# Kernel optimization log

Measured on AMD Instinct MI355X. Metric: run time of the kernel, lower is better.

## Reference

```python
import jax, jax.numpy as jnp
import numpy as np

N0, N1, N2, N3 = 65536, 16384, 4096, 1024
S = 9  # 3x3 kernel -> 9 selections (self + 8 directions)


def _edges(key, n):
    # each node has S incoming edges, one per selection
    src = jax.random.randint(key, (n * S,), 0, n)
    dst = jnp.repeat(jnp.arange(n), S)
    sel = jnp.tile(jnp.arange(S), n)
    return src, dst, sel


def setup_inputs() -> dict:
    key = jax.random.key(0)
    ks = jax.random.split(key, 40)
    inp = {}
    inp["x"] = jax.random.normal(ks[0], (N0, 3), jnp.float32)
    sizes = [N0, N1, N2, N3]
    for l, n in enumerate(sizes):
        src, dst, sel = _edges(ks[1 + l], n)
        inp[f"src{l}"] = src
        inp[f"dst{l}"] = dst
        inp[f"sel{l}"] = sel
        inp[f"interp{l}"] = jax.random.uniform(ks[5 + l], (n * S,), jnp.float32)
    inp["clus0"] = jnp.arange(N0) // 4
    inp["clus1"] = jnp.arange(N1) // 4
    inp["clus2"] = jnp.arange(N2) // 4
    dims = [(3, 3), (3, 64), (64, 64), (64, 128), (128, 128), (128, 256), (256, 256), (256, 256), (256, 256), (256, 512)]
    for i, (ci, co) in enumerate(dims):
        kw = ks[10 + 2 * i]
        kb = ks[11 + 2 * i]
        if i == 0:  # conv1 is kernel_size=1 -> single weight matrix
            inp["W1"] = jax.random.normal(kw, (ci, co), jnp.float32) / np.sqrt(ci).astype(np.float32)
        else:
            inp[f"W{i + 1}"] = jax.random.normal(kw, (S, ci, co), jnp.float32) / np.sqrt(S * ci).astype(np.float32)
        inp[f"b{i + 1}"] = jax.random.normal(kb, (co,), jnp.float32) * 0.01
    return inp


def _sel_conv(x, src, dst, sel, interp, W, b):
    # message = interp * x[src]; routed to (dst, selection) bucket; per-selection weight
    n = x.shape[0]
    msg = x[src] * interp[:, None]                                  # [E, Cin]
    agg = jax.ops.segment_sum(msg, dst * S + sel, num_segments=n * S)
    agg = agg.reshape(n, S, -1)                                     # [N, S, Cin]
    return jnp.einsum('nsi,sio->no', agg, W) + b


def reference(x, src0, dst0, sel0, interp0, src1, dst1, sel1, interp1,
              src2, dst2, sel2, interp2, src3, dst3, sel3, interp3,
              clus0, clus1, clus2,
              W1, b1, W2, b2, W3, b3, W4, b4, W5, b5,
              W6, b6, W7, b7, W8, b8, W9, b9, W10, b10):
    relu = jax.nn.relu
    out = x @ W1 + b1                                              # conv1 (1x1), no relu
    r11 = relu(_sel_conv(out, src0, dst0, sel0, interp0, W2, b2))
    r12 = relu(_sel_conv(r11, src0, dst0, sel0, interp0, W3, b3))
    p1 = jax.ops.segment_max(r12, clus0, num_segments=N1)
    r21 = relu(_sel_conv(p1, src1, dst1, sel1, interp1, W4, b4))
    r22 = relu(_sel_conv(r21, src1, dst1, sel1, interp1, W5, b5))
    p2 = jax.ops.segment_max(r22, clus1, num_segments=N2)
    r31 = relu(_sel_conv(p2, src2, dst2, sel2, interp2, W6, b6))
    r32 = relu(_sel_conv(r31, src2, dst2, sel2, interp2, W7, b7))
    r33 = relu(_sel_conv(r32, src2, dst2, sel2, interp2, W8, b8))
    r34 = relu(_sel_conv(r33, src2, dst2, sel2, interp2, W9, b9))
    p3 = jax.ops.segment_max(r34, clus2, num_segments=N3)
    r41 = relu(_sel_conv(p3, src3, dst3, sel3, interp3, W10, b10))
    return (r11, r12, p1, r21, r22, p2, r31, r32, r33, r34, p3, r41)
```

## Files before the change

### kernel.cpp

```cpp
#include <hip/hip_runtime.h>
#include <hip/hip_bf16.h>
#include <cstddef>


#define S9 9

typedef __attribute__((ext_vector_type(8))) _Float16 f16x8;
typedef __attribute__((ext_vector_type(4))) float f32x4;

__device__ __forceinline__ unsigned short f2h(float f) {
    _Float16 h = (_Float16)f;
    unsigned short u;
    __builtin_memcpy(&u, &h, 2);
    return u;
}

__device__ void wt_tile(const float* __restrict__ in, unsigned short* __restrict__ out,
                        int K, int N, int t, float (*sm)[33]) {
    const int ktiles = K >> 6, ntiles = N >> 5;
    const int per = ktiles * ntiles;
    const int s = t / per;
    const int rem = t - s * per;
    const int kt = rem % ktiles, nt = rem / ktiles;
    const int k0 = kt * 64, n0 = nt * 32;
    const float* ip = in + (size_t)s * K * N;
    unsigned short* op = out + (size_t)s * N * K;
    const int tx = threadIdx.x & 31;
    const int ty = threadIdx.x >> 5;
#pragma unroll
    for (int r = ty; r < 64; r += 8)
        sm[r][tx] = ip[(size_t)(k0 + r) * N + n0 + tx];
    __syncthreads();
#pragma unroll
    for (int r = ty; r < 32; r += 8) {
        unsigned v = (unsigned)f2h(sm[2 * tx][r]) |
                     ((unsigned)f2h(sm[2 * tx + 1][r]) << 16);
        *(unsigned*)&op[(size_t)(n0 + r) * K + k0 + 2 * tx] = v;
    }
}

__global__ __launch_bounds__(256) void wt_all(
    const float* __restrict__ W2, const float* __restrict__ W3,
    const float* __restrict__ W4, const float* __restrict__ W5,
    const float* __restrict__ W6, const float* __restrict__ W7,
    const float* __restrict__ W8, const float* __restrict__ W9,
    const float* __restrict__ W10,
    unsigned short* o2, unsigned short* o3, unsigned short* o4,
    unsigned short* o5, unsigned short* o6, unsigned short* o7,
    unsigned short* o8, unsigned short* o9, unsigned short* o10) {
    __shared__ float sm[64][33];
    int b = blockIdx.x;
    if (b == 0) {
        for (int idx = threadIdx.x; idx < 64 * 32; idx += 256) {
            const int n = idx >> 5, k = idx & 31;
            o2[n * 32 + k] = (k < 27) ? f2h(W2[k * 64 + n]) : (unsigned short)0;
        }
        return;
    }
    b -= 1;
    if (b < 18)  { wt_tile(W3,  o3,  64,  64,  b, sm); return; }  b -= 18;
    if (b < 36)  { wt_tile(W4,  o4,  64,  128, b, sm); return; }  b -= 36;
    if (b < 72)  { wt_tile(W5,  o5,  128, 128, b, sm); return; }  b -= 72;
    if (b < 144) { wt_tile(W6,  o6,  128, 256, b, sm); return; }  b -= 144;
    if (b < 288) { wt_tile(W7,  o7,  256, 256, b, sm); return; }  b -= 288;
    if (b < 288) { wt_tile(W8,  o8,  256, 256, b, sm); return; }  b -= 288;
    if (b < 288) { wt_tile(W9,  o9,  256, 256, b, sm); return; }  b -= 288;
    wt_tile(W10, o10, 256, 512, b, sm);
}

__global__ void pool4_dual(const float* __restrict__ in, float* __restrict__ outf,
                           _Float16* __restrict__ outh, int total4, int C4) {
    int idx = blockIdx.x * blockDim.x + threadIdx.x;
    if (idx >= total4) return;
    int j = idx / C4;
    int c4 = idx - j * C4;
    const float4* base = (const float4*)in;
    float4 a = base[(size_t)(4 * j + 0) * C4 + c4];
    float4 b = base[(size_t)(4 * j + 1) * C4 + c4];
    float4 c = base[(size_t)(4 * j + 2) * C4 + c4];
    float4 d = base[(size_t)(4 * j + 3) * C4 + c4];
    float4 m;
    m.x = fmaxf(fmaxf(a.x, b.x), fmaxf(c.x, d.x));
    m.y = fmaxf(fmaxf(a.y, b.y), fmaxf(c.y, d.y));
    m.z = fmaxf(fmaxf(a.z, b.z), fmaxf(c.z, d.z));
    m.w = fmaxf(fmaxf(a.w, b.w), fmaxf(c.w, d.w));
    ((float4*)outf)[(size_t)j * C4 + c4] = m;
    uint2 h;
    h.x = (unsigned)f2h(m.x) | ((unsigned)f2h(m.y) << 16);
    h.y = (unsigned)f2h(m.z) | ((unsigned)f2h(m.w) << 16);
    *(uint2*)&outh[((size_t)j * C4 + c4) * 4] = h;
}

template <int BM, int WR, int WC, int MR, int NR>
__global__ __launch_bounds__(256) void selconv_k27(
    const float* __restrict__ x, const int* __restrict__ src,
    const float* __restrict__ interp, const float* __restrict__ W1,
    const float* __restrict__ b1, const _Float16* __restrict__ Wt2,
    const float* __restrict__ bias, float* __restrict__ out,
    _Float16* __restrict__ outh) {
    constexpr int COUT = 64;
    constexpr int LDA = 40;
    __shared__ _Float16 As[BM * LDA];

    const int tid = threadIdx.x;
    const int wave = tid >> 6;
    const int lane = tid & 63;
    const int wr = wave / WC;
    const int wc = wave % WC;
    const int node0 = blockIdx.x * BM;
    const int lm = lane & 15;
    const int kq = lane >> 4;

    const float w00 = W1[0], w01 = W1[1], w02 = W1[2];
    const float w10 = W1[3], w11 = W1[4], w12 = W1[5];
    const float w20 = W1[6], w21 = W1[7], w22 = W1[8];
    const float c0 = b1[0], c1 = b1[1], c2 = b1[2];

    for (int c = tid; c < BM * 5; c += 256) {
        const int ln = c / 5;
        As[ln * LDA + 27 + (c - ln * 5)] = (_Float16)0.f;
    }
    for (int c = tid; c < BM * S9; c += 256) {
        const int ln = c / S9;
        const int s = c - ln * S9;
        const int e = (node0 + ln) * S9 + s;
        const float t = interp[e];
        const float* xr = &x[(size_t)src[e] * 3];
        const float x0 = xr[0], x1 = xr[1], x2 = xr[2];
        const float y0 = fmaf(x0, w00, fmaf(x1, w10, fmaf(x2, w20, c0)));
        const float y1 = fmaf(x0, w01, fmaf(x1, w11, fmaf(x2, w21, c1)));
        const float y2 = fmaf(x0, w02, fmaf(x1, w12, fmaf(x2, w22, c2)));
        As[ln * LDA + s * 3 + 0] = (_Float16)(t * y0);
        As[ln * LDA + s * 3 + 1] = (_Float16)(t * y1);
        As[ln * LDA + s * 3 + 2] = (_Float16)(t * y2);
    }
    __syncthreads();

    f32x4 acc[MR][NR];
    f16x8 bfr[NR];
#pragma unroll
    for (int f = 0; f < NR; ++f) {
        const int col = wc * NR * 16 + f * 16 + lm;
        bfr[f] = *(const f16x8*)(Wt2 + col * 32 + kq * 8);
        const float bv = bias[col];
#pragma unroll
        for (int i = 0; i < MR; ++i) {
            acc[i][f][0] = bv; acc[i][f][1] = bv; acc[i][f][2] = bv; acc[i][f][3] = bv;
        }
    }
#pragma unroll
    for (int i = 0; i < MR; ++i) {
        const f16x8 af =
            *(const f16x8*)&As[(wr * MR * 16 + i * 16 + lm) * LDA + kq * 8];
#pragma unroll
        for (int f = 0; f < NR; ++f)
            acc[i][f] = __builtin_amdgcn_mfma_f32_16x16x32_f16(af, bfr[f],
                                                               acc[i][f], 0, 0, 0);
    }

#pragma unroll
    for (int i = 0; i < MR; ++i)
#pragma unroll
        for (int f = 0; f < NR; ++f) {
            const int col = wc * NR * 16 + f * 16 + lm;
#pragma unroll
            for (int r = 0; r < 4; ++r) {
                const int row = node0 + wr * MR * 16 + i * 16 + kq * 4 + r;
                const float v = fmaxf(acc[i][f][r], 0.f);
                out[(size_t)row * COUT + col] = v;
                outh[(size_t)row * COUT + col] = (_Float16)v;
            }
        }
}

template <int CIN, int COUT, int BM, int BNC, int WR, int WC, int MR, int NR>
__global__ __launch_bounds__(256) void selconv_f16(
    const _Float16* __restrict__ xin, const int* __restrict__ src,
    const float* __restrict__ interp, const _Float16* __restrict__ Wt,
    const float* __restrict__ bias, float* __restrict__ out,
    _Float16* __restrict__ outh) {
    static_assert(WR * WC == 4, "4 waves");
    static_assert(WR * MR * 16 == BM, "BM mismatch");
    static_assert(WC * NR * 16 == BNC, "BNC mismatch");
    constexpr int KSTEPS = CIN / 32;
    constexpr int LDA = CIN + 8;
    constexpr int C8 = CIN / 8;
    constexpr int ITER = (BM * C8) / 256;
    static_assert((BM * C8) % 256 == 0, "staging divisibility");

    __shared__ _Float16 As[BM * LDA];

    const int tid = threadIdx.x;
    const int wave = tid >> 6;
    const int lane = tid & 63;
    const int wr = wave / WC;
    const int wc = wave % WC;
    const int node0 = blockIdx.x * BM;
    const int cb = blockIdx.y * BNC;
    const int lm = lane & 15;
    const int kq = lane >> 4;

    f32x4 acc[MR][NR];
#pragma unroll
    for (int f = 0; f < NR; ++f) {
        const float bv = bias[cb + wc * NR * 16 + f * 16 + lm];
#pragma unroll
        for (int i = 0; i < MR; ++i) {
            acc[i][f][0] = bv; acc[i][f][1] = bv; acc[i][f][2] = bv; acc[i][f][3] = bv;
        }
    }

    const _Float16* __restrict__ Wb =
        Wt + ((size_t)cb + wc * NR * 16 + lm) * CIN + kq * 8;

#pragma unroll 1
    for (int s = 0; s < S9; ++s) {
        int sidx[ITER];
        float ta[ITER];
#pragma unroll
        for (int i = 0; i < ITER; ++i) {
            const int c = tid + i * 256;
            const int ln = c / C8;
            const int e = (node0 + ln) * S9 + s;
            sidx[i] = src[e];
            ta[i] = interp[e];
        }
        f16x8 va[ITER];
#pragma unroll
        for (int i = 0; i < ITER; ++i) {
            const int c = tid + i * 256;
            const int c8 = c - (c / C8) * C8;
            va[i] = *(const f16x8*)&xin[(size_t)sidx[i] * CIN + c8 * 8];
        }
        f16x8 bfr[KSTEPS][NR];
        {
            const _Float16* __restrict__ Wbs = Wb + (size_t)s * COUT * CIN;
#pragma unroll
            for (int kk = 0; kk < KSTEPS; ++kk)
#pragma unroll
                for (int f = 0; f < NR; ++f)
                    bfr[kk][f] = *(const f16x8*)(Wbs + (size_t)f * 16 * CIN + kk * 32);
        }
        __syncthreads();
#pragma unroll
        for (int i = 0; i < ITER; ++i) {
            const int c = tid + i * 256;
            const int ln = c / C8;
            const int c8 = c - ln * C8;
            const _Float16 ht = (_Float16)ta[i];
            f16x8 r;
#pragma unroll
            for (int j = 0; j < 8; ++j) r[j] = va[i][j] * ht;
            *(f16x8*)&As[ln * LDA + c8 * 8] = r;
        }
        __syncthreads();
#pragma unroll
        for (int kk = 0; kk < KSTEPS; ++kk) {
            f16x8 af[MR];
#pragma unroll
            for (int i = 0; i < MR; ++i)
                af[i] = *(const f16x8*)&As[(wr * MR * 16 + i * 16 + lm) * LDA +
                                           kk * 32 + kq * 8];
#pragma unroll
            for (int i = 0; i < MR; ++i)
#pragma unroll
                for (int f = 0; f < NR; ++f)
                    acc[i][f] = __builtin_amdgcn_mfma_f32_16x16x32_f16(
                        af[i], bfr[kk][f], acc[i][f], 0, 0, 0);
        }
    }

#pragma unroll
    for (int i = 0; i < MR; ++i)
#pragma unroll
        for (int f = 0; f < NR; ++f) {
            const int col = cb + wc * NR * 16 + f * 16 + lm;
#pragma unroll
            for (int r = 0; r < 4; ++r) {
                const int row = node0 + wr * MR * 16 + i * 16 + kq * 4 + r;
                const float v = fmaxf(acc[i][f][r], 0.f);
                out[(size_t)row * COUT + col] = v;
                if (outh) outh[(size_t)row * COUT + col] = (_Float16)v;
            }
        }
}

extern "C" void kernel_launch(void* const* d_in, const int* in_sizes, int n_in,
                              void* d_out, int out_size, void* d_ws, size_t ws_size,
                              hipStream_t stream) {
    const float* x = (const float*)d_in[0];
    const int* src0 = (const int*)d_in[1];
    const float* interp0 = (const float*)d_in[4];
    const int* src1 = (const int*)d_in[5];
    const float* interp1 = (const float*)d_in[8];
    const int* src2 = (const int*)d_in[9];
    const float* interp2 = (const float*)d_in[12];
    const int* src3 = (const int*)d_in[13];
    const float* interp3 = (const float*)d_in[16];
    const float* W1 = (const float*)d_in[20];
    const float* b1 = (const float*)d_in[21];
    const float* W2 = (const float*)d_in[22];
    const float* b2 = (const float*)d_in[23];
    const float* W3 = (const float*)d_in[24];
    const float* b3 = (const float*)d_in[25];
    const float* W4 = (const float*)d_in[26];
    const float* b4 = (const float*)d_in[27];
    const float* W5 = (const float*)d_in[28];
    const float* b5 = (const float*)d_in[29];
    const float* W6 = (const float*)d_in[30];
    const float* b6 = (const float*)d_in[31];
    const float* W7 = (const float*)d_in[32];
    const float* b7 = (const float*)d_in[33];
    const float* W8 = (const float*)d_in[34];
    const float* b8 = (const float*)d_in[35];
    const float* W9 = (const float*)d_in[36];
    const float* b9 = (const float*)d_in[37];
    const float* W10 = (const float*)d_in[38];
    const float* b10 = (const float*)d_in[39];

    float* out = (float*)d_out;
    float* r11 = out;
    float* r12 = r11 + (size_t)65536 * 64;
    float* p1 = r12 + (size_t)65536 * 64;
    float* r21 = p1 + (size_t)16384 * 64;
    float* r22 = r21 + (size_t)16384 * 128;
    float* p2 = r22 + (size_t)16384 * 128;
    float* r31 = p2 + (size_t)4096 * 128;
    float* r32 = r31 + (size_t)4096 * 256;
    float* r33 = r32 + (size_t)4096 * 256;
    float* r34 = r33 + (size_t)4096 * 256;
    float* p3 = r34 + (size_t)4096 * 256;
    float* r41 = p3 + (size_t)1024 * 256;

    unsigned short* w16 = (unsigned short*)d_ws;
    unsigned short* Wt2 = w16;
    unsigned short* Wt3 = Wt2 + (size_t)64 * 32;
    unsigned short* Wt4 = Wt3 + (size_t)9 * 64 * 64;
    unsigned short* Wt5 = Wt4 + (size_t)9 * 128 * 64;
    unsigned short* Wt6 = Wt5 + (size_t)9 * 128 * 128;
    unsigned short* Wt7 = Wt6 + (size_t)9 * 256 * 128;
    unsigned short* Wt8 = Wt7 + (size_t)9 * 256 * 256;
    unsigned short* Wt9 = Wt8 + (size_t)9 * 256 * 256;
    unsigned short* Wt10 = Wt9 + (size_t)9 * 256 * 256;
    unsigned short* endw = Wt10 + (size_t)9 * 512 * 256;
    _Float16* a11 = (_Float16*)endw;
    _Float16* ap1 = a11 + (size_t)65536 * 64;
    _Float16* a21 = ap1 + (size_t)16384 * 64;
    _Float16* ap2 = a21 + (size_t)16384 * 128;
    _Float16* a31 = ap2 + (size_t)4096 * 128;
    _Float16* a32 = a31 + (size_t)4096 * 256;
    _Float16* a33 = a32 + (size_t)4096 * 256;
    _Float16* ap3 = a33 + (size_t)4096 * 256;

    wt_all<<<1711, 256, 0, stream>>>(W2, W3, W4, W5, W6, W7, W8, W9, W10,
                                     Wt2, Wt3, Wt4, Wt5, Wt6, Wt7, Wt8, Wt9, Wt10);

    selconv_k27<64, 2, 2, 2, 2><<<dim3(65536 / 64), 256, 0, stream>>>(
        x, src0, interp0, W1, b1, (const _Float16*)Wt2, b2, r11, a11);

    selconv_f16<64, 64, 64, 64, 2, 2, 2, 2><<<dim3(65536 / 64, 1), 256, 0, stream>>>(
        a11, src0, interp0, (const _Float16*)Wt3, b3, r12, nullptr);
    pool4_dual<<<(16384 * 16 + 255) / 256, 256, 0, stream>>>(r12, p1, ap1,
                                                             16384 * 16, 16);

    selconv_f16<64, 128, 32, 64, 2, 2, 1, 2><<<dim3(16384 / 32, 2), 256, 0, stream>>>(
        ap1, src1, interp1, (const _Float16*)Wt4, b4, r21, a21);
    selconv_f16<128, 128, 32, 64, 2, 2, 1, 2><<<dim3(16384 / 32, 2), 256, 0, stream>>>(
        a21, src1, interp1, (const _Float16*)Wt5, b5, r22, nullptr);
    pool4_dual<<<(4096 * 32 + 255) / 256, 256, 0, stream>>>(r22, p2, ap2,
                                                            4096 * 32, 32);

    selconv_f16<128, 256, 32, 64, 2, 2, 1, 2><<<dim3(4096 / 32, 4), 256, 0, stream>>>(
        ap2, src2, interp2, (const _Float16*)Wt6, b6, r31, a31);
    selconv_f16<256, 256, 32, 64, 2, 2, 1, 2><<<dim3(4096 / 32, 4), 256, 0, stream>>>(
        a31, src2, interp2, (const _Float16*)Wt7, b7, r32, a32);
    selconv_f16<256, 256, 32, 64, 2, 2, 1, 2><<<dim3(4096 / 32, 4), 256, 0, stream>>>(
        a32, src2, interp2, (const _Float16*)Wt8, b8, r33, a33);
    selconv_f16<256, 256, 32, 64, 2, 2, 1, 2><<<dim3(4096 / 32, 4), 256, 0, stream>>>(
        a33, src2, interp2, (const _Float16*)Wt9, b9, r34, nullptr);
    pool4_dual<<<(1024 * 64 + 255) / 256, 256, 0, stream>>>(r34, p3, ap3,
                                                            1024 * 64, 64);

    selconv_f16<256, 512, 16, 64, 1, 4, 1, 1><<<dim3(1024 / 16, 8), 256, 0, stream>>>(
        ap3, src3, interp3, (const _Float16*)Wt10, b10, r41, nullptr);
}
```

Measured before the change: 428.3 us.

## Gather MFMA A-operands directly from global and fuse max-pool into selconv epilogue

Each selconv kernel now loads the gathered, interp-scaled rows straight from global memory into MFMA A fragments, with src/interp indices preloaded per lane. This removes the shared-memory staging and both __syncthreads per selection. The max-pool over clusters of 4 is fused into the epilogue of the preceding conv, because each lane's 4 accumulator rows form one cluster; this drops the separate pool kernels and their re-read of the fp32 output. In exchange, columns split across waves or blocks re-gather the same rows redundantly, and the first layer switches to a 4x1 wave layout.

```diff
diff --git a/kernel.cpp b/kernel.cpp
--- a/kernel.cpp
+++ b/kernel.cpp
@@ -68,29 +68,6 @@
     wt_tile(W10, o10, 256, 512, b, sm);
 }
 
-__global__ void pool4_dual(const float* __restrict__ in, float* __restrict__ outf,
-                           _Float16* __restrict__ outh, int total4, int C4) {
-    int idx = blockIdx.x * blockDim.x + threadIdx.x;
-    if (idx >= total4) return;
-    int j = idx / C4;
-    int c4 = idx - j * C4;
-    const float4* base = (const float4*)in;
-    float4 a = base[(size_t)(4 * j + 0) * C4 + c4];
-    float4 b = base[(size_t)(4 * j + 1) * C4 + c4];
-    float4 c = base[(size_t)(4 * j + 2) * C4 + c4];
-    float4 d = base[(size_t)(4 * j + 3) * C4 + c4];
-    float4 m;
-    m.x = fmaxf(fmaxf(a.x, b.x), fmaxf(c.x, d.x));
-    m.y = fmaxf(fmaxf(a.y, b.y), fmaxf(c.y, d.y));
-    m.z = fmaxf(fmaxf(a.z, b.z), fmaxf(c.z, d.z));
-    m.w = fmaxf(fmaxf(a.w, b.w), fmaxf(c.w, d.w));
-    ((float4*)outf)[(size_t)j * C4 + c4] = m;
-    uint2 h;
-    h.x = (unsigned)f2h(m.x) | ((unsigned)f2h(m.y) << 16);
-    h.y = (unsigned)f2h(m.z) | ((unsigned)f2h(m.w) << 16);
-    *(uint2*)&outh[((size_t)j * C4 + c4) * 4] = h;
-}
-
 template <int BM, int WR, int WC, int MR, int NR>
 __global__ __launch_bounds__(256) void selconv_k27(
     const float* __restrict__ x, const int* __restrict__ src,
@@ -173,22 +150,17 @@
         }
 }
 
-template <int CIN, int COUT, int BM, int BNC, int WR, int WC, int MR, int NR>
-__global__ __launch_bounds__(256) void selconv_f16(
+template <int CIN, int COUT, int BM, int BNC, int WR, int WC, int MR, int NR,
+          bool POOL>
+__global__ __launch_bounds__(256) void selconv_dg(
     const _Float16* __restrict__ xin, const int* __restrict__ src,
     const float* __restrict__ interp, const _Float16* __restrict__ Wt,
     const float* __restrict__ bias, float* __restrict__ out,
-    _Float16* __restrict__ outh) {
+    float* __restrict__ poolf, _Float16* __restrict__ outh) {
     static_assert(WR * WC == 4, "4 waves");
     static_assert(WR * MR * 16 == BM, "BM mismatch");
     static_assert(WC * NR * 16 == BNC, "BNC mismatch");
     constexpr int KSTEPS = CIN / 32;
-    constexpr int LDA = CIN + 8;
-    constexpr int C8 = CIN / 8;
-    constexpr int ITER = (BM * C8) / 256;
-    static_assert((BM * C8) % 256 == 0, "staging divisibility");
-
-    __shared__ _Float16 As[BM * LDA];
 
     const int tid = threadIdx.x;
     const int wave = tid >> 6;
@@ -210,79 +182,74 @@
         }
     }
 
-    const _Float16* __restrict__ Wb =
+    int srows[MR][S9];
+    _Float16 ts[MR][S9];
+#pragma unroll
+    for (int i = 0; i < MR; ++i) {
+        const int ebase = (node0 + (wr * MR + i) * 16 + lm) * S9;
+#pragma unroll
+        for (int s = 0; s < S9; ++s) {
+            srows[i][s] = src[ebase + s];
+            ts[i][s] = (_Float16)interp[ebase + s];
+        }
+    }
+
+    const _Float16* __restrict__ Wcol =
         Wt + ((size_t)cb + wc * NR * 16 + lm) * CIN + kq * 8;
 
-#pragma unroll 1
+#pragma unroll
     for (int s = 0; s < S9; ++s) {
-        int sidx[ITER];
-        float ta[ITER];
-#pragma unroll
-        for (int i = 0; i < ITER; ++i) {
-            const int c = tid + i * 256;
-            const int ln = c / C8;
-            const int e = (node0 + ln) * S9 + s;
-            sidx[i] = src[e];
-            ta[i] = interp[e];
-        }
-        f16x8 va[ITER];
-#pragma unroll
-        for (int i = 0; i < ITER; ++i) {
-            const int c = tid + i * 256;
-            const int c8 = c - (c / C8) * C8;
-            va[i] = *(const f16x8*)&xin[(size_t)sidx[i] * CIN + c8 * 8];
-        }
-        f16x8 bfr[KSTEPS][NR];
-        {
-            const _Float16* __restrict__ Wbs = Wb + (size_t)s * COUT * CIN;
-#pragma unroll
-            for (int kk = 0; kk < KSTEPS; ++kk)
-#pragma unroll
-                for (int f = 0; f < NR; ++f)
-                    bfr[kk][f] = *(const f16x8*)(Wbs + (size_t)f * 16 * CIN + kk * 32);
-        }
-        __syncthreads();
-#pragma unroll
-        for (int i = 0; i < ITER; ++i) {
-            const int c = tid + i * 256;
-            const int ln = c / C8;
-            const int c8 = c - ln * C8;
-            const _Float16 ht = (_Float16)ta[i];
-            f16x8 r;
-#pragma unroll
-            for (int j = 0; j < 8; ++j) r[j] = va[i][j] * ht;
-            *(f16x8*)&As[ln * LDA + c8 * 8] = r;
-        }
-        __syncthreads();
+        const _Float16* __restrict__ Wbs = Wcol + (size_t)s * COUT * CIN;
 #pragma unroll
         for (int kk = 0; kk < KSTEPS; ++kk) {
+            f16x8 bf[NR];
+#pragma unroll
+            for (int f = 0; f < NR; ++f)
+                bf[f] = *(const f16x8*)(Wbs + (size_t)f * 16 * CIN + kk * 32);
             f16x8 af[MR];
 #pragma unroll
-            for (int i = 0; i < MR; ++i)
-                af[i] = *(const f16x8*)&As[(wr * MR * 16 + i * 16 + lm) * LDA +
-                                           kk * 32 + kq * 8];
+            for (int i = 0; i < MR; ++i) {
+                const f16x8 v = *(const f16x8*)(xin + (size_t)srows[i][s] * CIN +
+                                                kk * 32 + kq * 8);
+                const _Float16 t = ts[i][s];
+#pragma unroll
+                for (int j = 0; j < 8; ++j) af[i][j] = v[j] * t;
+            }
 #pragma unroll
             for (int i = 0; i < MR; ++i)
 #pragma unroll
                 for (int f = 0; f < NR; ++f)
                     acc[i][f] = __builtin_amdgcn_mfma_f32_16x16x32_f16(
-                        af[i], bfr[kk][f], acc[i][f], 0, 0, 0);
-        }
-    }
-
-#pragma unroll
-    for (int i = 0; i < MR; ++i)
+                        af[i], bf[f], acc[i][f], 0, 0, 0);
+        }
+    }
+
+#pragma unroll
+    for (int i = 0; i < MR; ++i) {
+        const int rowb = node0 + (wr * MR + i) * 16 + kq * 4;
 #pragma unroll
         for (int f = 0; f < NR; ++f) {
             const int col = cb + wc * NR * 16 + f * 16 + lm;
+            float v[4];
 #pragma unroll
             for (int r = 0; r < 4; ++r) {
-                const int row = node0 + wr * MR * 16 + i * 16 + kq * 4 + r;
-                const float v = fmaxf(acc[i][f][r], 0.f);
-                out[(size_t)row * COUT + col] = v;
-                if (outh) outh[(size_t)row * COUT + col] = (_Float16)v;
+                v[r] = fmaxf(acc[i][f][r], 0.f);
+                out[(size_t)(rowb + r) * COUT + col] = v[r];
             }
-        }
+            if constexpr (POOL) {
+                const float m = fmaxf(fmaxf(v[0], v[1]), fmaxf(v[2], v[3]));
+                const int prow = rowb >> 2;
+                poolf[(size_t)prow * COUT + col] = m;
+                outh[(size_t)prow * COUT + col] = (_Float16)m;
+            } else {
+                if (outh) {
+#pragma unroll
+                    for (int r = 0; r < 4; ++r)
+                        outh[(size_t)(rowb + r) * COUT + col] = (_Float16)v[r];
+                }
+            }
+        }
+    }
 }
 
 extern "C" void kernel_launch(void* const* d_in, const int* in_sizes, int n_in,
@@ -358,29 +325,31 @@
     selconv_k27<64, 2, 2, 2, 2><<<dim3(65536 / 64), 256, 0, stream>>>(
         x, src0, interp0, W1, b1, (const _Float16*)Wt2, b2, r11, a11);
 
-    selconv_f16<64, 64, 64, 64, 2, 2, 2, 2><<<dim3(65536 / 64, 1), 256, 0, stream>>>(
-        a11, src0, interp0, (const _Float16*)Wt3, b3, r12, nullptr);
-    pool4_dual<<<(16384 * 16 + 255) / 256, 256, 0, stream>>>(r12, p1, ap1,
-                                                             16384 * 16, 16);
-
-    selconv_f16<64, 128, 32, 64, 2, 2, 1, 2><<<dim3(16384 / 32, 2), 256, 0, stream>>>(
-        ap1, src1, interp1, (const _Float16*)Wt4, b4, r21, a21);
-    selconv_f16<128, 128, 32, 64, 2, 2, 1, 2><<<dim3(16384 / 32, 2), 256, 0, stream>>>(
-        a21, src1, interp1, (const _Float16*)Wt5, b5, r22, nullptr);
-    pool4_dual<<<(4096 * 32 + 255) / 256, 256, 0, stream>>>(r22, p2, ap2,
-                                                            4096 * 32, 32);
-
-    selconv_f16<128, 256, 32, 64, 2, 2, 1, 2><<<dim3(4096 / 32, 4), 256, 0, stream>>>(
-        ap2, src2, interp2, (const _Float16*)Wt6, b6, r31, a31);
-    selconv_f16<256, 256, 32, 64, 2, 2, 1, 2><<<dim3(4096 / 32, 4), 256, 0, stream>>>(
-        a31, src2, interp2, (const _Float16*)Wt7, b7, r32, a32);
-    selconv_f16<256, 256, 32, 64, 2, 2, 1, 2><<<dim3(4096 / 32, 4), 256, 0, stream>>>(
-        a32, src2, interp2, (const _Float16*)Wt8, b8, r33, a33);
-    selconv_f16<256, 256, 32, 64, 2, 2, 1, 2><<<dim3(4096 / 32, 4), 256, 0, stream>>>(
-        a33, src2, interp2, (const _Float16*)Wt9, b9, r34, nullptr);
-    pool4_dual<<<(1024 * 64 + 255) / 256, 256, 0, stream>>>(r34, p3, ap3,
-                                                            1024 * 64, 64);
-
-    selconv_f16<256, 512, 16, 64, 1, 4, 1, 1><<<dim3(1024 / 16, 8), 256, 0, stream>>>(
-        ap3, src3, interp3, (const _Float16*)Wt10, b10, r41, nullptr);
-}
+    selconv_dg<64, 64, 64, 64, 4, 1, 1, 4, true>
+        <<<dim3(65536 / 64, 1), 256, 0, stream>>>(
+            a11, src0, interp0, (const _Float16*)Wt3, b3, r12, p1, ap1);
+
+    selconv_dg<64, 128, 32, 64, 2, 2, 1, 2, false>
+        <<<dim3(16384 / 32, 2), 256, 0, stream>>>(
+            ap1, src1, interp1, (const _Float16*)Wt4, b4, r21, nullptr, a21);
+    selconv_dg<128, 128, 32, 64, 2, 2, 1, 2, true>
+        <<<dim3(16384 / 32, 2), 256, 0, stream>>>(
+            a21, src1, interp1, (const _Float16*)Wt5, b5, r22, p2, ap2);
+
+    selconv_dg<128, 256, 32, 64, 2, 2, 1, 2, false>
+        <<<dim3(4096 / 32, 4), 256, 0, stream>>>(
+            ap2, src2, interp2, (const _Float16*)Wt6, b6, r31, nullptr, a31);
+    selconv_dg<256, 256, 32, 64, 2, 2, 1, 2, false>
+        <<<dim3(4096 / 32, 4), 256, 0, stream>>>(
+            a31, src2, interp2, (const _Float16*)Wt7, b7, r32, nullptr, a32);
+    selconv_dg<256, 256, 32, 64, 2, 2, 1, 2, false>
+        <<<dim3(4096 / 32, 4), 256, 0, stream>>>(
+            a32, src2, interp2, (const _Float16*)Wt8, b8, r33, nullptr, a33);
+    selconv_dg<256, 256, 32, 64, 2, 2, 1, 2, true>
+        <<<dim3(4096 / 32, 4), 256, 0, stream>>>(
+            a33, src2, interp2, (const _Float16*)Wt9, b9, r34, p3, ap3);
+
+    selconv_dg<256, 512, 16, 64, 1, 4, 1, 1, false>
+        <<<dim3(1024 / 16, 8), 256, 0, stream>>>(
+            ap3, src3, interp3, (const _Float16*)Wt10, b10, r41, nullptr, nullptr);
+}
```

Result: slower. 507.1 us (+18.4%).
